# Kernel tuning notes

Measured on AMD Instinct MI355X. Metric: run time of the kernel, lower is better.

Reference implementation:

```python
import jax, jax.numpy as jnp
import numpy as np

N_GRAPHS = 500
CHAIN = 200
D_STATE = 64
HID = 128
NEG_SLOPE = 0.2  # PyG GATConv default


def setup_inputs() -> dict:
    key = jax.random.key(0)
    ks = jax.random.split(key, 9)
    N = N_GRAPHS * CHAIN
    # batched bidirectional chain graphs (as in create_chain_graph_batch)
    off = np.arange(N_GRAPHS, dtype=np.int32) * CHAIN
    a = (off[:, None] + np.arange(CHAIN - 1, dtype=np.int32)[None, :]).ravel()
    b = a + 1
    edge_index = jnp.asarray(np.stack([np.concatenate([a, b]), np.concatenate([b, a])]), dtype=jnp.int32)
    x = jax.random.normal(ks[0], (N, D_STATE), jnp.float32)
    s1 = 1.0 / np.sqrt(D_STATE)
    W1 = jax.random.normal(ks[1], (D_STATE, 2 * HID), jnp.float32) * s1
    att_src1 = jax.random.normal(ks[2], (2, HID), jnp.float32) * (1.0 / np.sqrt(HID))
    att_dst1 = jax.random.normal(ks[3], (2, HID), jnp.float32) * (1.0 / np.sqrt(HID))
    b1 = jnp.zeros((2 * HID,), jnp.float32)
    s2 = 1.0 / np.sqrt(2 * HID)
    W2 = jax.random.normal(ks[4], (2 * HID, HID), jnp.float32) * s2
    att_src2 = jax.random.normal(ks[5], (1, HID), jnp.float32) * (1.0 / np.sqrt(HID))
    att_dst2 = jax.random.normal(ks[6], (1, HID), jnp.float32) * (1.0 / np.sqrt(HID))
    b2 = jnp.zeros((HID,), jnp.float32)
    return {"x": x, "edge_index": edge_index, "W1": W1, "att_src1": att_src1,
            "att_dst1": att_dst1, "b1": b1, "W2": W2, "att_src2": att_src2,
            "att_dst2": att_dst2, "b2": b2}


def gat_conv(x, src, dst, W, att_src, att_dst, bias, concat):
    # PyG GATConv: per-head linear, additive attention, segment softmax over dst
    N = x.shape[0]
    H, C = att_src.shape
    h = (x @ W).reshape(N, H, C)                          # [N,H,C]
    a_s = (h * att_src).sum(-1)                           # [N,H]
    a_d = (h * att_dst).sum(-1)                           # [N,H]
    logits = jax.nn.leaky_relu(a_s[src] + a_d[dst], NEG_SLOPE)  # [E,H]
    m = jax.ops.segment_max(logits, dst, num_segments=N)
    e = jnp.exp(logits - m[dst])
    s = jax.ops.segment_sum(e, dst, num_segments=N)
    alpha = e / (s[dst] + 1e-16)                          # [E,H]
    out = jax.ops.segment_sum(h[src] * alpha[:, :, None], dst, num_segments=N)  # [N,H,C]
    out = out.reshape(N, H * C) if concat else out.mean(axis=1)
    return out + bias


def reference(x, edge_index, W1, att_src1, att_dst1, b1, W2, att_src2, att_dst2, b2):
    N = x.shape[0]
    loop = jnp.arange(N, dtype=edge_index.dtype)
    src = jnp.concatenate([edge_index[0], loop])  # add_self_loops=True (PyG default)
    dst = jnp.concatenate([edge_index[1], loop])
    h = gat_conv(x, src, dst, W1, att_src1, att_dst1, b1, concat=True)
    h = jax.nn.gelu(h, approximate=False)  # torch F.gelu default = exact erf
    h = gat_conv(h, src, dst, W2, att_src2, att_dst2, b2, concat=False)
    return jax.nn.gelu(h, approximate=False)
```

## Files before the change

kernel.cpp:

```cpp
#include <hip/hip_runtime.h>
#include <hip/hip_bf16.h>

#define NG 500
#define CH 200
#define NN (NG*CH)
#define DS 64
#define HDIM 128
#define C1 256
#define NEG_SLOPE 0.2f
#define GB 1563

typedef unsigned short ushort_t;
typedef __attribute__((ext_vector_type(8))) short bf16x8;
typedef __attribute__((ext_vector_type(4))) float f32x4;

__device__ __forceinline__ float us2f(ushort_t u){
  union { unsigned int i; float f; } v; v.i = ((unsigned int)u) << 16; return v.f;
}
__device__ __forceinline__ ushort_t f2us(float f){
  union { float f; unsigned int i; } v; v.f = f;
  unsigned int x = v.i;
  return (ushort_t)((x + 0x7fffu + ((x >> 16) & 1u)) >> 16);
}
__device__ __forceinline__ unsigned int cvt_pk_bf16(float a, float b){
  unsigned int r;
  asm("v_cvt_pk_bf16_f32 %0, %1, %2" : "=v"(r) : "v"(a), "v"(b));
  return r;
}
__device__ __forceinline__ float lrelu(float v){ return v > 0.f ? v : NEG_SLOPE * v; }
__device__ __forceinline__ float gelu_fast(float x){
  float x2 = x * x;
  float zn = x * fmaf(-0.0713548163f, x2, -1.5957691216f);
  float e  = __expf(zn);
  return x * __builtin_amdgcn_rcpf(1.f + e);
}

__global__ void probe_dtype(const void* __restrict__ x, int* __restrict__ flag){
  __shared__ int cnt;
  if (threadIdx.x == 0) cnt = 0;
  __syncthreads();
  const ushort_t* p = (const ushort_t*)x;
  int local = 0;
  for (int i = threadIdx.x; i < 8192; i += 256) {
    float v = us2f(p[i]);
    if (!(fabsf(v) < 100.f)) local++;
  }
  atomicAdd(&cnt, local);
  __syncthreads();
  if (threadIdx.x == 0) flag[0] = (cnt > 16) ? 1 : 0;
}

__global__ void prep_w(const int* __restrict__ flag,
                       const void* W1, const void* as1, const void* ad1, const void* b1,
                       const void* W2, const void* as2, const void* ad2, const void* b2,
                       ushort_t* w1t, ushort_t* w2t,
                       float* b1f, float* b2f,
                       ushort_t* wsd1, ushort_t* wsd2)
{
  const bool F = flag[0] != 0;
  int i = blockIdx.x * 256 + threadIdx.x;
  #define LD(p, j) (F ? ((const float*)(p))[j] : us2f(((const ushort_t*)(p))[j]))
  if (i < 16384)      { int k = i >> 8, n = i & 255; w1t[n*64  + k] = f2us(LD(W1, i)); }
  else if (i < 49152) { int j = i - 16384, k = j >> 7, n = j & 127; w2t[n*256 + k] = f2us(LD(W2, j)); }
  else if (i < 49408) { b1f[i-49152] = LD(b1, i-49152); }
  else if (i < 49536) { b2f[i-49408] = LD(b2, i-49408); }
  else if (i < 53632) {
    int j = i - 49536, dot = j >> 4, lsub = j & 15;
    int k = dot >> 2, c = dot & 3, head = c >> 1;
    const void* av = (c & 1) ? ad1 : as1;
    float s = 0.f;
    #pragma unroll
    for (int jj = 0; jj < 8; jj++) {
      int cc = lsub*8 + jj;
      s += LD(W1, k*256 + head*128 + cc) * LD(av, head*128 + cc);
    }
    s += __shfl_xor(s, 1, 64); s += __shfl_xor(s, 2, 64);
    s += __shfl_xor(s, 4, 64); s += __shfl_xor(s, 8, 64);
    if (lsub == 0) {
      ushort_t hi = f2us(s);
      wsd1[c*64 + k] = hi;
      wsd1[(c+4)*64 + k] = f2us(s - us2f(hi));
    }
  }
  else if (i < 61824) {
    int j = i - 53632, dot = j >> 4, lsub = j & 15;
    int k = dot >> 1, c = dot & 1;
    const void* av = c ? ad2 : as2;
    float s = 0.f;
    #pragma unroll
    for (int jj = 0; jj < 8; jj++) {
      int cc = lsub*8 + jj;
      s += LD(W2, k*128 + cc) * LD(av, cc);
    }
    s += __shfl_xor(s, 1, 64); s += __shfl_xor(s, 2, 64);
    s += __shfl_xor(s, 4, 64); s += __shfl_xor(s, 8, 64);
    if (lsub == 0) {
      ushort_t hi = f2us(s);
      wsd2[c*256 + k] = hi;
      wsd2[(c+2)*256 + k] = f2us(s - us2f(hi));
    }
  }
  else if (i < 62336) { wsd1[512  + (i - 61824)] = 0; }
  else if (i < 65408) { wsd2[1024 + (i - 62336)] = 0; }
  #undef LD
}

__global__ __launch_bounds__(512, 4) void fused(
    const int* __restrict__ flag, const void* __restrict__ x,
    const ushort_t* __restrict__ w1t, const ushort_t* __restrict__ w2t,
    const ushort_t* __restrict__ wsd1, const ushort_t* __restrict__ wsd2,
    const float* __restrict__ b1f, const float* __restrict__ b2f,
    void* __restrict__ out)
{
  __shared__ ushort_t lds[17952];
  __shared__ float scratch[800];
  ushort_t* As  = lds;
  ushort_t* g1L = lds;

  const int t  = threadIdx.x;
  const int m0 = blockIdx.x * 64;
  const int l = t & 63, w = t >> 6;
  const int ln = l & 15, quad = l >> 4;
  const bool F = flag[0] != 0;

  #pragma unroll
  for (int i = 0; i < 3; i++) {
    int q = t + i*512;
    if (q >= 1280) break;
    int r = q >> 4, off = (q & 15) * 4;
    int gr = m0 - 2 + r;
    if (r < 68 && gr >= 0 && gr < NN) {
      if (F) {
        float4 xv = *(const float4*)(&((const float*)x)[(size_t)gr*DS + off]);
        uint2 u; u.x = cvt_pk_bf16(xv.x, xv.y); u.y = cvt_pk_bf16(xv.z, xv.w);
        *(uint2*)(&As[r*72 + off]) = u;
      } else {
        *(ushort4*)(&As[r*72 + off]) = *(const ushort4*)(&((const ushort_t*)x)[(size_t)gr*DS + off]);
      }
    } else {
      ushort4 z = {0,0,0,0};
      *(ushort4*)(&As[r*72 + off]) = z;
    }
  }

  f32x4 acc[5][2];
  #pragma unroll
  for (int mi = 0; mi < 5; mi++)
    #pragma unroll
    for (int nj = 0; nj < 2; nj++) acc[mi][nj] = (f32x4){0.f,0.f,0.f,0.f};
  f32x4 acc_att[5];
  #pragma unroll
  for (int mi = 0; mi < 5; mi++) acc_att[mi] = (f32x4){0.f,0.f,0.f,0.f};

  __syncthreads();
  #pragma unroll
  for (int ks = 0; ks < 2; ks++) {
    const int kk = ks*32 + quad*8;
    bf16x8 a[5], b[2];
    #pragma unroll
    for (int nj = 0; nj < 2; nj++)
      b[nj] = *(const bf16x8*)(&w1t[(w*32 + nj*16 + ln)*64 + kk]);
    #pragma unroll
    for (int mi = 0; mi < 5; mi++) a[mi] = *(const bf16x8*)(&As[(mi*16 + ln)*72 + kk]);
    #pragma unroll
    for (int mi = 0; mi < 5; mi++)
      #pragma unroll
      for (int nj = 0; nj < 2; nj++)
        acc[mi][nj] = __builtin_amdgcn_mfma_f32_16x16x32_bf16(a[mi], b[nj], acc[mi][nj], 0, 0, 0);
    if (w == 0) {
      bf16x8 batt = *(const bf16x8*)(&wsd1[ln*64 + kk]);
      #pragma unroll
      for (int mi = 0; mi < 5; mi++)
        acc_att[mi] = __builtin_amdgcn_mfma_f32_16x16x32_bf16(a[mi], batt, acc_att[mi], 0, 0, 0);
    }
  }

  if (w == 0) {
    #pragma unroll
    for (int mi = 0; mi < 5; mi++)
      #pragma unroll
      for (int r = 0; r < 4; r++) {
        float v = acc_att[mi][r];
        float vc = v + __shfl(v, (l + 4) & 63, 64);
        int row = mi*16 + quad*4 + r;
        if (ln < 4 && row < 68) scratch[ln*68 + row] = vc;
      }
  }
  __syncthreads();

  if (t < 132) {
    int hh = (t >= 66) ? 1 : 0;
    int n  = t - 66*hh;
    int gj = m0 - 1 + n;
    int p  = gj % CH;
    const float* Sa = &scratch[(2*hh)*68];
    const float* Da = &scratch[(2*hh+1)*68];
    float ad = Da[n+1], as_s = Sa[n+1], as_l = Sa[n], as_r = Sa[n+2];
    bool hl = p > 0, hr = p < CH-1;
    float zs = lrelu(as_s + ad);
    float zl = hl ? lrelu(as_l + ad) : -1e30f;
    float zr = hr ? lrelu(as_r + ad) : -1e30f;
    float mx = fmaxf(zs, fmaxf(zl, zr));
    float el = hl ? __expf(zl - mx) : 0.f;
    float es = __expf(zs - mx);
    float er = hr ? __expf(zr - mx) : 0.f;
    float inv = __builtin_amdgcn_rcpf(el + es + er + 1e-16f);
    scratch[272 + n*8 + hh*4 + 0] = el*inv;
    scratch[272 + n*8 + hh*4 + 1] = es*inv;
    scratch[272 + n*8 + hh*4 + 2] = er*inv;
  }
  __syncthreads();

  {
    float b1v[2];
    #pragma unroll
    for (int nj = 0; nj < 2; nj++) b1v[nj] = b1f[w*32 + nj*16 + ln];
    if (t < 128) {
      int rr = (t < 64) ? 0 : 67;
      int c4 = (t & 63) * 4;
      ushort4 z = {0,0,0,0};
      *(ushort4*)(&g1L[rr*264 + c4]) = z;
    }
    const int head = w >> 2;
    #pragma unroll
    for (int mi = 0; mi < 5; mi++) {
      const int mip = (mi < 4) ? mi+1 : 4;
      const int mim = (mi > 0) ? mi-1 : 0;
      float hp3[2], hm0[2];
      #pragma unroll
      for (int nj = 0; nj < 2; nj++) {
        float up_a = __shfl(acc[mi ][nj][0], (l+16)&63, 64);
        float up_b = __shfl(acc[mip][nj][0], (l+16)&63, 64);
        float dn_a = __shfl(acc[mi ][nj][3], (l-16)&63, 64);
        float dn_b = __shfl(acc[mim][nj][3], (l-16)&63, 64);
        hp3[nj] = (quad < 3) ? up_a : up_b;
        hm0[nj] = (quad > 0) ? dn_a : dn_b;
      }
      #pragma unroll
      for (int r = 0; r < 4; r++) {
        int row = mi*16 + quad*4 + r;
        if (row >= 1 && row <= 66) {
          float4 av = *(const float4*)(&scratch[272 + (row-1)*8 + head*4]);
          float o[2];
          #pragma unroll
          for (int nj = 0; nj < 2; nj++) {
            float self = acc[mi][nj][r];
            float hm = (r > 0) ? acc[mi][nj][r-1] : hm0[nj];
            float hp = (r < 3) ? acc[mi][nj][r+1] : hp3[nj];
            o[nj] = gelu_fast(av.y*self + av.x*hm + av.z*hp + b1v[nj]);
          }
          unsigned int u01 = cvt_pk_bf16(o[0], o[1]);
          ushort_t* base = &g1L[row*264 + w*32 + ln];
          base[0]  = (ushort_t)u01;
          base[16] = (ushort_t)(u01 >> 16);
        }
      }
    }
  }
  __syncthreads();

  f32x4 acc2[5];
  #pragma unroll
  for (int mi = 0; mi < 5; mi++) acc2[mi] = (f32x4){0.f,0.f,0.f,0.f};
  f32x4 acc2_att[5];
  #pragma unroll
  for (int mi = 0; mi < 5; mi++) acc2_att[mi] = (f32x4){0.f,0.f,0.f,0.f};

  #pragma unroll
  for (int ck = 0; ck < 4; ck++) {
    #pragma unroll
    for (int ks = 0; ks < 2; ks++) {
      const int kk = ks*32 + quad*8;
      bf16x8 a2[5];
      #pragma unroll
      for (int mi = 0; mi < 5; mi++) {
        int ar = mi*16 + ln;
        if (mi == 4) ar = (ar < 67) ? ar : 67;
        a2[mi] = *(const bf16x8*)(&g1L[ar*264 + ck*64 + kk]);
      }
      bf16x8 b = *(const bf16x8*)(&w2t[(w*16 + ln)*256 + ck*64 + kk]);
      #pragma unroll
      for (int mi = 0; mi < 5; mi++)
        acc2[mi] = __builtin_amdgcn_mfma_f32_16x16x32_bf16(a2[mi], b, acc2[mi], 0, 0, 0);
      if (w == ck) {
        bf16x8 batt2 = *(const bf16x8*)(&wsd2[ln*256 + ck*64 + kk]);
        #pragma unroll
        for (int mi = 0; mi < 5; mi++)
          acc2_att[mi] = __builtin_amdgcn_mfma_f32_16x16x32_bf16(a2[mi], batt2, acc2_att[mi], 0, 0, 0);
      }
    }
  }

  if (w < 4) {
    #pragma unroll
    for (int mi = 0; mi < 5; mi++)
      #pragma unroll
      for (int r = 0; r < 4; r++) {
        float v = acc2_att[mi][r];
        float vc = v + __shfl(v, (l + 2) & 63, 64);
        int row = mi*16 + quad*4 + r;
        if (ln < 2 && row < 68) scratch[(w*2 + ln)*68 + row] = vc;
      }
  }
  __syncthreads();

  if (t < 64) {
    int gi = m0 + t;
    if (gi < NN) {
      int p = gi % CH;
      float ad = 0.f, as_s = 0.f, as_l = 0.f, as_r = 0.f;
      #pragma unroll
      for (int ww = 0; ww < 4; ww++) {
        as_s += scratch[(ww*2)*68 + t+2];
        as_l += scratch[(ww*2)*68 + t+1];
        as_r += scratch[(ww*2)*68 + t+3];
        ad   += scratch[(ww*2+1)*68 + t+2];
      }
      bool hl = p > 0, hr = p < CH-1;
      float zs = lrelu(as_s + ad);
      float zl = hl ? lrelu(as_l + ad) : -1e30f;
      float zr = hr ? lrelu(as_r + ad) : -1e30f;
      float mx = fmaxf(zs, fmaxf(zl, zr));
      float el = hl ? __expf(zl - mx) : 0.f;
      float es = __expf(zs - mx);
      float er = hr ? __expf(zr - mx) : 0.f;
      float inv = __builtin_amdgcn_rcpf(el + es + er + 1e-16f);
      scratch[544 + t*4 + 0] = el*inv;
      scratch[544 + t*4 + 1] = es*inv;
      scratch[544 + t*4 + 2] = er*inv;
    }
  }
  __syncthreads();

  {
    float b2v = b2f[w*16 + ln];
    #pragma unroll
    for (int mi = 0; mi < 5; mi++) {
      const int mip = (mi < 4) ? mi+1 : 4;
      const int mim = (mi > 0) ? mi-1 : 0;
      float hp3, hm0;
      {
        float up_a = __shfl(acc2[mi ][0], (l+16)&63, 64);
        float up_b = __shfl(acc2[mip][0], (l+16)&63, 64);
        float dn_a = __shfl(acc2[mi ][3], (l-16)&63, 64);
        float dn_b = __shfl(acc2[mim][3], (l-16)&63, 64);
        hp3 = (quad < 3) ? up_a : up_b;
        hm0 = (quad > 0) ? dn_a : dn_b;
      }
      #pragma unroll
      for (int r = 0; r < 4; r++) {
        int row = mi*16 + quad*4 + r;
        if (row >= 2 && row <= 65) {
          int n = row - 2;
          int gi = m0 + n;
          if (gi < NN) {
            float4 av = *(const float4*)(&scratch[544 + n*4]);
            float self = acc2[mi][r];
            float hm = (r > 0) ? acc2[mi][r-1] : hm0;
            float hp = (r < 3) ? acc2[mi][r+1] : hp3;
            float o = gelu_fast(av.y*self + av.x*hm + av.z*hp + b2v);
            int c2 = w*16 + ln;
            if (F) ((float*)out)[(size_t)gi*HDIM + c2] = o;
            else   ((ushort_t*)out)[(size_t)gi*HDIM + c2] = f2us(o);
          }
        }
      }
    }
  }
}

extern "C" void kernel_launch(void* const* d_in, const int* in_sizes, int n_in,
                              void* d_out, int out_size, void* d_ws, size_t ws_size,
                              hipStream_t stream)
{
  const void* x   = d_in[0];
  const void* W1  = d_in[2];
  const void* as1 = d_in[3];
  const void* ad1 = d_in[4];
  const void* b1  = d_in[5];
  const void* W2  = d_in[6];
  const void* as2 = d_in[7];
  const void* ad2 = d_in[8];
  const void* b2  = d_in[9];

  char* w = (char*)d_ws;
  size_t off = 0;
  int* flag = (int*)w;                       off += 256;
  ushort_t* w1t = (ushort_t*)(w + off);      off += 64 * 256 * 2;
  ushort_t* w2t = (ushort_t*)(w + off);      off += 256 * 128 * 2;
  float* b1f    = (float*)(w + off);         off += 256 * 4;
  float* b2f    = (float*)(w + off);         off += 128 * 4;
  ushort_t* wsd1 = (ushort_t*)(w + off);     off += 16 * 64 * 2;
  ushort_t* wsd2 = (ushort_t*)(w + off);     off += 16 * 256 * 2;

  probe_dtype<<<1, 256, 0, stream>>>(x, flag);
  prep_w<<<256, 256, 0, stream>>>(flag, W1, as1, ad1, b1, W2, as2, ad2, b2,
                                  w1t, w2t, b1f, b2f, wsd1, wsd2);
  fused<<<GB, 512, 0, stream>>>(flag, x, w1t, w2t, wsd1, wsd2, b1f, b2f, d_out);
}
```

Before: 158.9 us.

## Split warps into 2x4 M/N grid and compute attention softmax in registers

Reorganizes the 8 warps from an N-only split (each warp covering all 5 row tiles) into a 2x4 grid: two row groups of 3 overlapping 16-row tiles, each warp doing 4 (layer 1) or 2 (layer 2) column tiles. Every warp now computes the attention-score MFMA itself and gets the per-row source/destination scores through cross-lane shuffles. This drops the scratch LDS array, the single-warp softmax phases and two barriers per layer. The cost is redundant attention MFMAs in every warp, overlapping halo tiles computed twice, and more accumulator registers per thread.

```diff
diff --git a/kernel.cpp b/kernel.cpp
--- a/kernel.cpp
+++ b/kernel.cpp
@@ -113,7 +113,6 @@
     void* __restrict__ out)
 {
   __shared__ ushort_t lds[17952];
-  __shared__ float scratch[800];
   ushort_t* As  = lds;
   ushort_t* g1L = lds;
 
@@ -121,7 +120,11 @@
   const int m0 = blockIdx.x * 64;
   const int l = t & 63, w = t >> 6;
   const int ln = l & 15, quad = l >> 4;
+  const int mg = w >> 2, wn = w & 3;
+  const int head = wn >> 1;
+  const int qb = l & 48;
   const bool F = flag[0] != 0;
+  const int pm0 = m0 % CH;
 
   #pragma unroll
   for (int i = 0; i < 3; i++) {
@@ -143,226 +146,219 @@
     }
   }
 
-  f32x4 acc[5][2];
-  #pragma unroll
-  for (int mi = 0; mi < 5; mi++)
-    #pragma unroll
-    for (int nj = 0; nj < 2; nj++) acc[mi][nj] = (f32x4){0.f,0.f,0.f,0.f};
-  f32x4 acc_att[5];
-  #pragma unroll
-  for (int mi = 0; mi < 5; mi++) acc_att[mi] = (f32x4){0.f,0.f,0.f,0.f};
+  f32x4 acc[3][4];
+  #pragma unroll
+  for (int mu = 0; mu < 3; mu++)
+    #pragma unroll
+    for (int nj = 0; nj < 4; nj++) acc[mu][nj] = (f32x4){0.f,0.f,0.f,0.f};
+  f32x4 acc_att[3];
+  #pragma unroll
+  for (int mu = 0; mu < 3; mu++) acc_att[mu] = (f32x4){0.f,0.f,0.f,0.f};
 
   __syncthreads();
   #pragma unroll
   for (int ks = 0; ks < 2; ks++) {
     const int kk = ks*32 + quad*8;
-    bf16x8 a[5], b[2];
-    #pragma unroll
-    for (int nj = 0; nj < 2; nj++)
-      b[nj] = *(const bf16x8*)(&w1t[(w*32 + nj*16 + ln)*64 + kk]);
-    #pragma unroll
-    for (int mi = 0; mi < 5; mi++) a[mi] = *(const bf16x8*)(&As[(mi*16 + ln)*72 + kk]);
-    #pragma unroll
-    for (int mi = 0; mi < 5; mi++)
-      #pragma unroll
-      for (int nj = 0; nj < 2; nj++)
-        acc[mi][nj] = __builtin_amdgcn_mfma_f32_16x16x32_bf16(a[mi], b[nj], acc[mi][nj], 0, 0, 0);
-    if (w == 0) {
-      bf16x8 batt = *(const bf16x8*)(&wsd1[ln*64 + kk]);
-      #pragma unroll
-      for (int mi = 0; mi < 5; mi++)
-        acc_att[mi] = __builtin_amdgcn_mfma_f32_16x16x32_bf16(a[mi], batt, acc_att[mi], 0, 0, 0);
-    }
-  }
-
-  if (w == 0) {
-    #pragma unroll
-    for (int mi = 0; mi < 5; mi++)
+    bf16x8 a[3], b[4], batt;
+    #pragma unroll
+    for (int nj = 0; nj < 4; nj++)
+      b[nj] = *(const bf16x8*)(&w1t[(wn*64 + nj*16 + ln)*64 + kk]);
+    batt = *(const bf16x8*)(&wsd1[ln*64 + kk]);
+    #pragma unroll
+    for (int mu = 0; mu < 3; mu++)
+      a[mu] = *(const bf16x8*)(&As[((mg*2+mu)*16 + ln)*72 + kk]);
+    #pragma unroll
+    for (int mu = 0; mu < 3; mu++) {
+      #pragma unroll
+      for (int nj = 0; nj < 4; nj++)
+        acc[mu][nj] = __builtin_amdgcn_mfma_f32_16x16x32_bf16(a[mu], b[nj], acc[mu][nj], 0, 0, 0);
+      acc_att[mu] = __builtin_amdgcn_mfma_f32_16x16x32_bf16(a[mu], batt, acc_att[mu], 0, 0, 0);
+    }
+  }
+  __syncthreads();
+
+  float sv[3][4], dv[3][4];
+  {
+    const int cs = 2*head, cd = 2*head + 1;
+    #pragma unroll
+    for (int mu = 0; mu < 3; mu++)
       #pragma unroll
       for (int r = 0; r < 4; r++) {
-        float v = acc_att[mi][r];
-        float vc = v + __shfl(v, (l + 4) & 63, 64);
-        int row = mi*16 + quad*4 + r;
-        if (ln < 4 && row < 68) scratch[ln*68 + row] = vc;
-      }
-  }
-  __syncthreads();
-
-  if (t < 132) {
-    int hh = (t >= 66) ? 1 : 0;
-    int n  = t - 66*hh;
-    int gj = m0 - 1 + n;
-    int p  = gj % CH;
-    const float* Sa = &scratch[(2*hh)*68];
-    const float* Da = &scratch[(2*hh+1)*68];
-    float ad = Da[n+1], as_s = Sa[n+1], as_l = Sa[n], as_r = Sa[n+2];
-    bool hl = p > 0, hr = p < CH-1;
-    float zs = lrelu(as_s + ad);
-    float zl = hl ? lrelu(as_l + ad) : -1e30f;
-    float zr = hr ? lrelu(as_r + ad) : -1e30f;
-    float mx = fmaxf(zs, fmaxf(zl, zr));
-    float el = hl ? __expf(zl - mx) : 0.f;
-    float es = __expf(zs - mx);
-    float er = hr ? __expf(zr - mx) : 0.f;
-    float inv = __builtin_amdgcn_rcpf(el + es + er + 1e-16f);
-    scratch[272 + n*8 + hh*4 + 0] = el*inv;
-    scratch[272 + n*8 + hh*4 + 1] = es*inv;
-    scratch[272 + n*8 + hh*4 + 2] = er*inv;
-  }
-  __syncthreads();
+        float v = acc_att[mu][r];
+        sv[mu][r] = __shfl(v, qb + cs, 64) + __shfl(v, qb + cs + 4, 64);
+        dv[mu][r] = __shfl(v, qb + cd, 64) + __shfl(v, qb + cd + 4, 64);
+      }
+  }
 
   {
-    float b1v[2];
-    #pragma unroll
-    for (int nj = 0; nj < 2; nj++) b1v[nj] = b1f[w*32 + nj*16 + ln];
+    const int RLO = mg ? 34 : 1, RHI = mg ? 66 : 33;
+    float b1v[4];
+    #pragma unroll
+    for (int nj = 0; nj < 4; nj++) b1v[nj] = b1f[wn*64 + nj*16 + ln];
     if (t < 128) {
       int rr = (t < 64) ? 0 : 67;
       int c4 = (t & 63) * 4;
       ushort4 z = {0,0,0,0};
       *(ushort4*)(&g1L[rr*264 + c4]) = z;
     }
-    const int head = w >> 2;
-    #pragma unroll
-    for (int mi = 0; mi < 5; mi++) {
-      const int mip = (mi < 4) ? mi+1 : 4;
-      const int mim = (mi > 0) ? mi-1 : 0;
-      float hp3[2], hm0[2];
-      #pragma unroll
-      for (int nj = 0; nj < 2; nj++) {
-        float up_a = __shfl(acc[mi ][nj][0], (l+16)&63, 64);
-        float up_b = __shfl(acc[mip][nj][0], (l+16)&63, 64);
-        float dn_a = __shfl(acc[mi ][nj][3], (l-16)&63, 64);
-        float dn_b = __shfl(acc[mim][nj][3], (l-16)&63, 64);
+    #pragma unroll
+    for (int mu = 0; mu < 3; mu++) {
+      const int mup = (mu < 2) ? mu+1 : 2;
+      const int mum = (mu > 0) ? mu-1 : 0;
+      const int muG = mg*2 + mu;
+      float hp3[4], hm0[4];
+      #pragma unroll
+      for (int nj = 0; nj < 4; nj++) {
+        float up_a = __shfl(acc[mu ][nj][0], (l+16)&63, 64);
+        float up_b = __shfl(acc[mup][nj][0], (l+16)&63, 64);
+        float dn_a = __shfl(acc[mu ][nj][3], (l-16)&63, 64);
+        float dn_b = __shfl(acc[mum][nj][3], (l-16)&63, 64);
         hp3[nj] = (quad < 3) ? up_a : up_b;
         hm0[nj] = (quad > 0) ? dn_a : dn_b;
       }
+      float sN3_a = __shfl(sv[mu ][0], (l+16)&63, 64);
+      float sN3_b = __shfl(sv[mup][0], (l+16)&63, 64);
+      float sP0_a = __shfl(sv[mu ][3], (l-16)&63, 64);
+      float sP0_b = __shfl(sv[mum][3], (l-16)&63, 64);
+      float sN3 = (quad < 3) ? sN3_a : sN3_b;
+      float sP0 = (quad > 0) ? sP0_a : sP0_b;
       #pragma unroll
       for (int r = 0; r < 4; r++) {
-        int row = mi*16 + quad*4 + r;
-        if (row >= 1 && row <= 66) {
-          float4 av = *(const float4*)(&scratch[272 + (row-1)*8 + head*4]);
-          float o[2];
-          #pragma unroll
-          for (int nj = 0; nj < 2; nj++) {
-            float self = acc[mi][nj][r];
-            float hm = (r > 0) ? acc[mi][nj][r-1] : hm0[nj];
-            float hp = (r < 3) ? acc[mi][nj][r+1] : hp3[nj];
-            o[nj] = gelu_fast(av.y*self + av.x*hm + av.z*hp + b1v[nj]);
-          }
-          unsigned int u01 = cvt_pk_bf16(o[0], o[1]);
-          ushort_t* base = &g1L[row*264 + w*32 + ln];
-          base[0]  = (ushort_t)u01;
-          base[16] = (ushort_t)(u01 >> 16);
+        int row = muG*16 + quad*4 + r;
+        if (row < RLO || row > RHI) continue;
+        float s_o = sv[mu][r], d_o = dv[mu][r];
+        float sP = (r > 0) ? sv[mu][r-1] : sP0;
+        float sN = (r < 3) ? sv[mu][r+1] : sN3;
+        int p = pm0 + row - 2;
+        if (p < 0) p += CH;
+        if (p >= CH) p -= CH;
+        bool hl = p > 0, hr = p < CH-1;
+        float zs = lrelu(s_o + d_o);
+        float zl = hl ? lrelu(sP + d_o) : -1e30f;
+        float zr = hr ? lrelu(sN + d_o) : -1e30f;
+        float mx = fmaxf(zs, fmaxf(zl, zr));
+        float el = hl ? __expf(zl - mx) : 0.f;
+        float es = __expf(zs - mx);
+        float er = hr ? __expf(zr - mx) : 0.f;
+        float inv = __builtin_amdgcn_rcpf(el + es + er + 1e-16f);
+        el *= inv; es *= inv; er *= inv;
+        float o[4];
+        #pragma unroll
+        for (int nj = 0; nj < 4; nj++) {
+          float self = acc[mu][nj][r];
+          float hm = (r > 0) ? acc[mu][nj][r-1] : hm0[nj];
+          float hp = (r < 3) ? acc[mu][nj][r+1] : hp3[nj];
+          o[nj] = gelu_fast(es*self + el*hm + er*hp + b1v[nj]);
         }
-      }
-    }
-  }
-  __syncthreads();
-
-  f32x4 acc2[5];
-  #pragma unroll
-  for (int mi = 0; mi < 5; mi++) acc2[mi] = (f32x4){0.f,0.f,0.f,0.f};
-  f32x4 acc2_att[5];
-  #pragma unroll
-  for (int mi = 0; mi < 5; mi++) acc2_att[mi] = (f32x4){0.f,0.f,0.f,0.f};
+        unsigned int u01 = cvt_pk_bf16(o[0], o[1]);
+        unsigned int u23 = cvt_pk_bf16(o[2], o[3]);
+        ushort_t* base = &g1L[row*264 + wn*64 + ln];
+        base[0]  = (ushort_t)u01; base[16] = (ushort_t)(u01 >> 16);
+        base[32] = (ushort_t)u23; base[48] = (ushort_t)(u23 >> 16);
+      }
+    }
+  }
+  __syncthreads();
+
+  f32x4 acc2[3][2];
+  #pragma unroll
+  for (int mu = 0; mu < 3; mu++)
+    #pragma unroll
+    for (int nj = 0; nj < 2; nj++) acc2[mu][nj] = (f32x4){0.f,0.f,0.f,0.f};
+  f32x4 acc2_att[3];
+  #pragma unroll
+  for (int mu = 0; mu < 3; mu++) acc2_att[mu] = (f32x4){0.f,0.f,0.f,0.f};
 
   #pragma unroll
   for (int ck = 0; ck < 4; ck++) {
     #pragma unroll
     for (int ks = 0; ks < 2; ks++) {
       const int kk = ks*32 + quad*8;
-      bf16x8 a2[5];
-      #pragma unroll
-      for (int mi = 0; mi < 5; mi++) {
-        int ar = mi*16 + ln;
-        if (mi == 4) ar = (ar < 67) ? ar : 67;
-        a2[mi] = *(const bf16x8*)(&g1L[ar*264 + ck*64 + kk]);
-      }
-      bf16x8 b = *(const bf16x8*)(&w2t[(w*16 + ln)*256 + ck*64 + kk]);
-      #pragma unroll
-      for (int mi = 0; mi < 5; mi++)
-        acc2[mi] = __builtin_amdgcn_mfma_f32_16x16x32_bf16(a2[mi], b, acc2[mi], 0, 0, 0);
-      if (w == ck) {
-        bf16x8 batt2 = *(const bf16x8*)(&wsd2[ln*256 + ck*64 + kk]);
+      bf16x8 a2[3];
+      #pragma unroll
+      for (int mu = 0; mu < 3; mu++) {
+        int ar = (mg*2+mu)*16 + ln;
+        ar = (ar < 67) ? ar : 67;
+        a2[mu] = *(const bf16x8*)(&g1L[ar*264 + ck*64 + kk]);
+      }
+      bf16x8 b0 = *(const bf16x8*)(&w2t[(wn*32 +      ln)*256 + ck*64 + kk]);
+      bf16x8 b1 = *(const bf16x8*)(&w2t[(wn*32 + 16 + ln)*256 + ck*64 + kk]);
+      bf16x8 batt2 = *(const bf16x8*)(&wsd2[ln*256 + ck*64 + kk]);
+      #pragma unroll
+      for (int mu = 0; mu < 3; mu++) {
+        acc2[mu][0] = __builtin_amdgcn_mfma_f32_16x16x32_bf16(a2[mu], b0, acc2[mu][0], 0, 0, 0);
+        acc2[mu][1] = __builtin_amdgcn_mfma_f32_16x16x32_bf16(a2[mu], b1, acc2[mu][1], 0, 0, 0);
+        acc2_att[mu] = __builtin_amdgcn_mfma_f32_16x16x32_bf16(a2[mu], batt2, acc2_att[mu], 0, 0, 0);
+      }
+    }
+  }
+
+  float sv2[3][4], dv2[3][4];
+  #pragma unroll
+  for (int mu = 0; mu < 3; mu++)
+    #pragma unroll
+    for (int r = 0; r < 4; r++) {
+      float v = acc2_att[mu][r];
+      sv2[mu][r] = __shfl(v, qb + 0, 64) + __shfl(v, qb + 2, 64);
+      dv2[mu][r] = __shfl(v, qb + 1, 64) + __shfl(v, qb + 3, 64);
+    }
+
+  {
+    const int OLO = mg ? 34 : 2, OHI = mg ? 65 : 33;
+    float b2v[2];
+    #pragma unroll
+    for (int nj = 0; nj < 2; nj++) b2v[nj] = b2f[wn*32 + nj*16 + ln];
+    #pragma unroll
+    for (int mu = 0; mu < 3; mu++) {
+      const int mup = (mu < 2) ? mu+1 : 2;
+      const int mum = (mu > 0) ? mu-1 : 0;
+      const int muG = mg*2 + mu;
+      float hp3[2], hm0[2];
+      #pragma unroll
+      for (int nj = 0; nj < 2; nj++) {
+        float up_a = __shfl(acc2[mu ][nj][0], (l+16)&63, 64);
+        float up_b = __shfl(acc2[mup][nj][0], (l+16)&63, 64);
+        float dn_a = __shfl(acc2[mu ][nj][3], (l-16)&63, 64);
+        float dn_b = __shfl(acc2[mum][nj][3], (l-16)&63, 64);
+        hp3[nj] = (quad < 3) ? up_a : up_b;
+        hm0[nj] = (quad > 0) ? dn_a : dn_b;
+      }
+      float sN3_a = __shfl(sv2[mu ][0], (l+16)&63, 64);
+      float sN3_b = __shfl(sv2[mup][0], (l+16)&63, 64);
+      float sP0_a = __shfl(sv2[mu ][3], (l-16)&63, 64);
+      float sP0_b = __shfl(sv2[mum][3], (l-16)&63, 64);
+      float sN3 = (quad < 3) ? sN3_a : sN3_b;
+      float sP0 = (quad > 0) ? sP0_a : sP0_b;
+      #pragma unroll
+      for (int r = 0; r < 4; r++) {
+        int row = muG*16 + quad*4 + r;
+        if (row < OLO || row > OHI) continue;
+        int gi = m0 + row - 2;
+        if (gi >= NN) continue;
+        float s_o = sv2[mu][r], d_o = dv2[mu][r];
+        float sP = (r > 0) ? sv2[mu][r-1] : sP0;
+        float sN = (r < 3) ? sv2[mu][r+1] : sN3;
+        int p = pm0 + row - 2;
+        if (p >= CH) p -= CH;
+        bool hl = p > 0, hr = p < CH-1;
+        float zs = lrelu(s_o + d_o);
+        float zl = hl ? lrelu(sP + d_o) : -1e30f;
+        float zr = hr ? lrelu(sN + d_o) : -1e30f;
+        float mx = fmaxf(zs, fmaxf(zl, zr));
+        float el = hl ? __expf(zl - mx) : 0.f;
+        float es = __expf(zs - mx);
+        float er = hr ? __expf(zr - mx) : 0.f;
+        float inv = __builtin_amdgcn_rcpf(el + es + er + 1e-16f);
+        el *= inv; es *= inv; er *= inv;
         #pragma unroll
-        for (int mi = 0; mi < 5; mi++)
-          acc2_att[mi] = __builtin_amdgcn_mfma_f32_16x16x32_bf16(a2[mi], batt2, acc2_att[mi], 0, 0, 0);
-      }
-    }
-  }
-
-  if (w < 4) {
-    #pragma unroll
-    for (int mi = 0; mi < 5; mi++)
-      #pragma unroll
-      for (int r = 0; r < 4; r++) {
-        float v = acc2_att[mi][r];
-        float vc = v + __shfl(v, (l + 2) & 63, 64);
-        int row = mi*16 + quad*4 + r;
-        if (ln < 2 && row < 68) scratch[(w*2 + ln)*68 + row] = vc;
-      }
-  }
-  __syncthreads();
-
-  if (t < 64) {
-    int gi = m0 + t;
-    if (gi < NN) {
-      int p = gi % CH;
-      float ad = 0.f, as_s = 0.f, as_l = 0.f, as_r = 0.f;
-      #pragma unroll
-      for (int ww = 0; ww < 4; ww++) {
-        as_s += scratch[(ww*2)*68 + t+2];
-        as_l += scratch[(ww*2)*68 + t+1];
-        as_r += scratch[(ww*2)*68 + t+3];
-        ad   += scratch[(ww*2+1)*68 + t+2];
-      }
-      bool hl = p > 0, hr = p < CH-1;
-      float zs = lrelu(as_s + ad);
-      float zl = hl ? lrelu(as_l + ad) : -1e30f;
-      float zr = hr ? lrelu(as_r + ad) : -1e30f;
-      float mx = fmaxf(zs, fmaxf(zl, zr));
-      float el = hl ? __expf(zl - mx) : 0.f;
-      float es = __expf(zs - mx);
-      float er = hr ? __expf(zr - mx) : 0.f;
-      float inv = __builtin_amdgcn_rcpf(el + es + er + 1e-16f);
-      scratch[544 + t*4 + 0] = el*inv;
-      scratch[544 + t*4 + 1] = es*inv;
-      scratch[544 + t*4 + 2] = er*inv;
-    }
-  }
-  __syncthreads();
-
-  {
-    float b2v = b2f[w*16 + ln];
-    #pragma unroll
-    for (int mi = 0; mi < 5; mi++) {
-      const int mip = (mi < 4) ? mi+1 : 4;
-      const int mim = (mi > 0) ? mi-1 : 0;
-      float hp3, hm0;
-      {
-        float up_a = __shfl(acc2[mi ][0], (l+16)&63, 64);
-        float up_b = __shfl(acc2[mip][0], (l+16)&63, 64);
-        float dn_a = __shfl(acc2[mi ][3], (l-16)&63, 64);
-        float dn_b = __shfl(acc2[mim][3], (l-16)&63, 64);
-        hp3 = (quad < 3) ? up_a : up_b;
-        hm0 = (quad > 0) ? dn_a : dn_b;
-      }
-      #pragma unroll
-      for (int r = 0; r < 4; r++) {
-        int row = mi*16 + quad*4 + r;
-        if (row >= 2 && row <= 65) {
-          int n = row - 2;
-          int gi = m0 + n;
-          if (gi < NN) {
-            float4 av = *(const float4*)(&scratch[544 + n*4]);
-            float self = acc2[mi][r];
-            float hm = (r > 0) ? acc2[mi][r-1] : hm0;
-            float hp = (r < 3) ? acc2[mi][r+1] : hp3;
-            float o = gelu_fast(av.y*self + av.x*hm + av.z*hp + b2v);
-            int c2 = w*16 + ln;
-            if (F) ((float*)out)[(size_t)gi*HDIM + c2] = o;
-            else   ((ushort_t*)out)[(size_t)gi*HDIM + c2] = f2us(o);
-          }
+        for (int nj = 0; nj < 2; nj++) {
+          float self = acc2[mu][nj][r];
+          float hm = (r > 0) ? acc2[mu][nj][r-1] : hm0[nj];
+          float hp = (r < 3) ? acc2[mu][nj][r+1] : hp3[nj];
+          float o = gelu_fast(es*self + el*hm + er*hp + b2v[nj]);
+          int c2 = wn*32 + nj*16 + ln;
+          if (F) ((float*)out)[(size_t)gi*HDIM + c2] = o;
+          else   ((ushort_t*)out)[(size_t)gi*HDIM + c2] = f2us(o);
         }
       }
     }
```

Result: slower. 194.1 us (+22.1%).
